# Optimization experiments

Hardware: AMD Instinct MI355X
Metric: run time of the kernel (lower is better)

The kernel has to match this reference:

```python
import jax, jax.numpy as jnp
import numpy as np

N, E = 100000, 1600000
IN_CH, HID, HEADS, OUT_CH = 128, 32, 2, 40
NEG_SLOPE = 0.2
BN_EPS = 1e-5


def _param(key, shape, scale=0.1):
    return scale * jax.random.normal(key, shape, dtype=jnp.float32)


def setup_inputs() -> dict:
    key = jax.random.key(0)
    ks = jax.random.split(key, 24)
    x = jax.random.normal(ks[0], (N, IN_CH), dtype=jnp.float32)
    edge_index = jax.random.randint(ks[1], (2, E), 0, N, dtype=jnp.int32)
    d0 = HEADS * HID  # 64
    inp = {
        'x': x, 'edge_index': edge_index,
        # conv0: in 128 -> 32 per head, concat -> 64
        'W0': _param(ks[2], (IN_CH, HEADS * HID)),
        'as0': _param(ks[3], (HEADS, HID)), 'ad0': _param(ks[4], (HEADS, HID)),
        'b0': jnp.zeros((d0,), jnp.float32),
        'g0': jnp.ones((d0,), jnp.float32), 'bt0': jnp.zeros((d0,), jnp.float32),
        # conv1: 64 -> 32 per head, concat -> 64
        'W1': _param(ks[5], (d0, HEADS * HID)),
        'as1': _param(ks[6], (HEADS, HID)), 'ad1': _param(ks[7], (HEADS, HID)),
        'b1': jnp.zeros((d0,), jnp.float32),
        'g1': jnp.ones((d0,), jnp.float32), 'bt1': jnp.zeros((d0,), jnp.float32),
        # conv2: 64 -> 40 per head, mean over heads -> 40
        'W2': _param(ks[8], (d0, HEADS * OUT_CH)),
        'as2': _param(ks[9], (HEADS, OUT_CH)), 'ad2': _param(ks[10], (HEADS, OUT_CH)),
        'b2': jnp.zeros((OUT_CH,), jnp.float32),
    }
    return inp


def gat_conv(x, src, dst, W, a_src, a_dst, bias, out_ch, concat):
    n = x.shape[0]
    h = (x @ W).reshape(n, HEADS, out_ch)            # [N,H,C]
    alpha_src = jnp.sum(h * a_src, axis=-1)          # [N,H]
    alpha_dst = jnp.sum(h * a_dst, axis=-1)          # [N,H]
    e = jax.nn.leaky_relu(alpha_src[src] + alpha_dst[dst], NEG_SLOPE)  # [E,H]
    # softmax over incoming edges per destination node (self loops guarantee >=1 edge)
    m = jax.ops.segment_max(e, dst, num_segments=n)
    e = jnp.exp(e - m[dst])
    s = jax.ops.segment_sum(e, dst, num_segments=n)
    alpha = e / s[dst]                                # [E,H]
    msg = h[src] * alpha[:, :, None]                  # [E,H,C]
    out = jax.ops.segment_sum(msg, dst, num_segments=n)  # [N,H,C]
    out = out.reshape(n, HEADS * out_ch) if concat else out.mean(axis=1)
    return out + bias


def batch_norm(x, gamma, beta):
    mu = jnp.mean(x, axis=0)
    var = jnp.mean(jnp.square(x - mu), axis=0)
    return gamma * (x - mu) * jax.lax.rsqrt(var + BN_EPS) + beta


def reference(x, edge_index, W0, as0, ad0, b0, g0, bt0,
              W1, as1, ad1, b1, g1, bt1, W2, as2, ad2, b2):
    n = x.shape[0]
    loops = jnp.arange(n, dtype=edge_index.dtype)
    src = jnp.concatenate([edge_index[0], loops])
    dst = jnp.concatenate([edge_index[1], loops])
    h = gat_conv(x, src, dst, W0, as0, ad0, b0, HID, True)
    h = jax.nn.elu(batch_norm(h, g0, bt0))
    h = gat_conv(h, src, dst, W1, as1, ad1, b1, HID, True)
    h = jax.nn.elu(batch_norm(h, g1, bt1))
    return gat_conv(h, src, dst, W2, as2, ad2, b2, OUT_CH, False)
```

## Files before the change

kernel.cpp:

```cpp
#include <hip/hip_runtime.h>
#include <hip/hip_bf16.h>
#include <math.h>


#define NNODES 100000
#define NEDGES 1600000
#define ENTOT  (NEDGES + NNODES)
#define NEG_SLOPE 0.2f
#define BN_EPS 1e-5f

#define NRANGE 8
#define RSIZE  (NNODES/NRANGE)
#define BCAP   262144
#define PBLK   2048
#define NB2    32

typedef unsigned short u16;
typedef unsigned int u32;
typedef unsigned long long u64;
typedef __attribute__((ext_vector_type(8))) short short8;
typedef __attribute__((ext_vector_type(4))) float f32x4;

__device__ __forceinline__ float b2f(u16 u){ union{u32 i; float f;} v; v.i=((u32)u)<<16; return v.f; }
__device__ __forceinline__ u16 f2b(float x){ __hip_bfloat16 b=__float2bfloat16(x); return *(u16*)&b; }
__device__ __forceinline__ float ldf(const void* p, int i, int f){
  return f ? ((const float*)p)[i] : b2f(((const u16*)p)[i]);
}

__global__ void k_detect(const u16* __restrict__ x, int* __restrict__ flag){
  __shared__ int bad;
  if(threadIdx.x==0) bad=0;
  __syncthreads();
  int cnt=0;
  for(int i=threadIdx.x;i<4096;i+=256){
    u16 v = x[2*i];
    int ex = (v>>7)&0xff;
    if(ex==0xff || (ex==0 && (v&0x7fff)!=0)) cnt++;
  }
  atomicAdd(&bad,cnt);
  __syncthreads();
  if(threadIdx.x==0) flag[0] = (bad>4)?1:0;
}

__global__ __launch_bounds__(256) void k_part2(
    const int* __restrict__ ei, int* __restrict__ gptr, u32* __restrict__ bkt){
  __shared__ int lcnt[NRANGE], gbase[NRANGE];
  int t=threadIdx.x;
  if(t<NRANGE) lcnt[t]=0;
  __syncthreads();
  const int CH=(ENTOT+PBLK-1)/PBLK;
  int beg=blockIdx.x*CH, end=beg+CH; if(end>ENTOT) end=ENTOT;
  int nd[4], ns[4], nr[4], ne=0;
  for(int i=beg+t; i<end; i+=256){
    int d=(i<NEDGES)? ei[NEDGES+i] : (i-NEDGES);
    int s=(i<NEDGES)? ei[i] : d;
    nd[ne]=d; ns[ne]=s; ne++;
  }
  #pragma unroll 4
  for(int k=0;k<ne;k++) nr[k]=atomicAdd(&lcnt[nd[k]/RSIZE],1);
  __syncthreads();
  if(t<NRANGE) gbase[t]=atomicAdd(&gptr[t],lcnt[t]);
  __syncthreads();
  #pragma unroll 4
  for(int k=0;k<ne;k++){
    int r=nd[k]/RSIZE;
    u32 e = ((u32)(nd[k]-r*RSIZE)<<17) | (u32)ns[k];
    __builtin_nontemporal_store(e, &bkt[(size_t)r*BCAP + gbase[r] + nr[k]]);
  }
}

__global__ __launch_bounds__(256) void k_hist4(
    const u32* __restrict__ bkt, const int* __restrict__ gptr, int* __restrict__ lhist){
  __shared__ int lh[RSIZE];
  int t=threadIdx.x;
  for(int i=t;i<RSIZE;i+=256) lh[i]=0;
  __syncthreads();
  int r = blockIdx.x & (NRANGE-1);
  int c = blockIdx.x >> 3;
  int n = gptr[r];
  int per=(n+NB2-1)/NB2;
  int beg=c*per, end=beg+per; if(end>n) end=n;
  const u32* bp = bkt + (size_t)r*BCAP;
  for(int i=beg+t;i<end;i+=256) atomicAdd(&lh[bp[i]>>17],1);
  __syncthreads();
  int* out = lhist + (size_t)(r*NB2+c)*RSIZE;
  for(int i=t;i<RSIZE;i+=256) out[i]=lh[i];
}

__global__ __launch_bounds__(256) void k_sumscan(int* __restrict__ lhist, int* __restrict__ cnt){
  int n = blockIdx.x*256 + threadIdx.x;
  if(n>=NNODES) return;
  int r = n/RSIZE, i = n - r*RSIZE;
  int* base = lhist + (size_t)r*NB2*RSIZE + i;
  int run=0;
  #pragma unroll 8
  for(int c=0;c<NB2;c++){
    int v = base[(size_t)c*RSIZE];
    base[(size_t)c*RSIZE] = run;
    run += v;
  }
  cnt[n]=run;
}

#define SCAN_M (NNODES+1)
#define SCAN_NB ((SCAN_M + 2047)/2048)

__global__ void k_scan_a(const int* __restrict__ cnt, int* __restrict__ bsum){
  __shared__ int red[256];
  int b=blockIdx.x, t=threadIdx.x;
  int base = b*2048 + t*8;
  int s=0;
  #pragma unroll
  for(int j=0;j<8;j++){ int idx=base+j; s += (idx<NNODES)? cnt[idx]:0; }
  red[t]=s; __syncthreads();
  for(int o=128;o>0;o>>=1){ if(t<o) red[t]+=red[t+o]; __syncthreads(); }
  if(t==0) bsum[b]=red[0];
}

__global__ void k_scan_b(int* bsum){
  if(threadIdx.x==0){
    int run=0;
    for(int i=0;i<SCAN_NB;i++){ int v=bsum[i]; bsum[i]=run; run+=v; }
  }
}

__global__ void k_scan_c(const int* __restrict__ cnt, const int* __restrict__ bsum,
                         int* __restrict__ row_ptr){
  __shared__ int lds[256];
  int b=blockIdx.x, t=threadIdx.x;
  int base=b*2048+t*8;
  int v[8]; int s=0;
  #pragma unroll
  for(int j=0;j<8;j++){ int idx=base+j; int x=(idx<NNODES)?cnt[idx]:0; v[j]=s; s+=x; }
  lds[t]=s; __syncthreads();
  for(int o=1;o<256;o<<=1){
    int other=0; if(t>=o) other=lds[t-o];
    __syncthreads();
    lds[t]+=other;
    __syncthreads();
  }
  int texcl = lds[t] - s;
  int off0 = bsum[b] + texcl;
  #pragma unroll
  for(int j=0;j<8;j++){ int idx=base+j; if(idx<SCAN_M) row_ptr[idx]=off0+v[j]; }
}

__global__ __launch_bounds__(256) void k_scatter4(
    const u32* __restrict__ bkt, const int* __restrict__ gptr,
    const int* __restrict__ row_ptr, const int* __restrict__ lhist,
    int* __restrict__ col){
  __shared__ int lofs[RSIZE];
  int t=threadIdx.x;
  int r = blockIdx.x & (NRANGE-1);
  int c = blockIdx.x >> 3;
  int lo = r*RSIZE;
  const int* cb = lhist + (size_t)(r*NB2+c)*RSIZE;
  for(int i=t;i<RSIZE;i+=256) lofs[i] = row_ptr[lo+i] + cb[i];
  __syncthreads();
  int n = gptr[r];
  int per=(n+NB2-1)/NB2;
  int beg=c*per, end=beg+per; if(end>n) end=n;
  const u32* bp = bkt + (size_t)r*BCAP;
  for(int i=beg+t;i<end;i+=256){
    u32 e=bp[i];
    int pos=atomicAdd(&lofs[e>>17],1);
    col[pos]=(int)(e & 0x1FFFF);
  }
}

template<int K, int OUTC, int HID, bool XEXT, bool BN>
__global__ __launch_bounds__(256) void k_gemm_mfma(
    const void* __restrict__ xin, const void* __restrict__ W,
    const void* __restrict__ avs, const void* __restrict__ avd,
    const float2* __restrict__ bnab,
    u16* __restrict__ hout, float* __restrict__ asrc, float* __restrict__ adst,
    const int* __restrict__ flagp)
{
  const int f = flagp[0];
  constexpr int KP = K+8;
  constexpr int RS = OUTC+8;
  constexpr int NT = OUTC/16;
  constexpr int KQ = K/32;
  __shared__ __align__(16) u16 WT[OUTC*KP];
  __shared__ __align__(16) u16 HROW[4*16*RS];
  __shared__ float AVb[2*OUTC];
  __shared__ float2 BB[K];
  int t=threadIdx.x;
  const u16* Wu=(const u16*)W; const float* Wf=(const float*)W;
  for(int i8=t*8; i8<K*OUTC; i8+=256*8){
    int k=i8/OUTC, c0=i8-k*OUTC;
    u16 w8[8];
    if(f){
      const float* wp=Wf+i8;
      float4 a=*(const float4*)wp, b=*(const float4*)(wp+4);
      w8[0]=f2b(a.x);w8[1]=f2b(a.y);w8[2]=f2b(a.z);w8[3]=f2b(a.w);
      w8[4]=f2b(b.x);w8[5]=f2b(b.y);w8[6]=f2b(b.z);w8[7]=f2b(b.w);
    } else {
      uint4 q=*(const uint4*)(Wu+i8);
      w8[0]=q.x&0xffff;w8[1]=q.x>>16;w8[2]=q.y&0xffff;w8[3]=q.y>>16;
      w8[4]=q.z&0xffff;w8[5]=q.z>>16;w8[6]=q.w&0xffff;w8[7]=q.w>>16;
    }
    #pragma unroll
    for(int u=0;u<8;u++) WT[(c0+u)*KP + k] = w8[u];
  }
  for(int idx=t; idx<2*OUTC; idx+=256)
    AVb[idx] = (idx<OUTC)? ldf(avs,idx,f) : ldf(avd,idx-OUTC,f);
  if(BN) for(int idx=t; idx<K; idx+=256) BB[idx]=bnab[idx];
  __syncthreads();

  int wv=t>>6, lane=t&63;
  int m=lane&15, quad=lane>>4;
  int grow0 = blockIdx.x*64 + wv*16;
  int growA = grow0 + m;
  bool avalid = growA < NNODES;
  int growC = avalid ? growA : 0;

  f32x4 acc[NT] = {};
  #pragma unroll
  for(int kq=0;kq<KQ;kq++){
    int k0 = kq*32 + quad*8;
    union{ u32 u[4]; short8 s8; } A;
    if(XEXT && f==1){
      const float* xr=(const float*)xin + (size_t)growC*K + k0;
      float4 p=*(const float4*)xr, q=*(const float4*)(xr+4);
      A.u[0]=f2b(p.x)|((u32)f2b(p.y)<<16);
      A.u[1]=f2b(p.z)|((u32)f2b(p.w)<<16);
      A.u[2]=f2b(q.x)|((u32)f2b(q.y)<<16);
      A.u[3]=f2b(q.z)|((u32)f2b(q.w)<<16);
    } else {
      uint4 q=*(const uint4*)((const u16*)xin + (size_t)growC*K + k0);
      A.u[0]=q.x; A.u[1]=q.y; A.u[2]=q.z; A.u[3]=q.w;
    }
    if(BN){
      #pragma unroll
      for(int j=0;j<4;j++){
        float lo=b2f(A.u[j]&0xffff), hi=b2f(A.u[j]>>16);
        float2 c1=BB[k0+2*j], c2=BB[k0+2*j+1];
        lo=c1.x*lo+c1.y; lo = lo>0.f? lo : __expf(lo)-1.f;
        hi=c2.x*hi+c2.y; hi = hi>0.f? hi : __expf(hi)-1.f;
        A.u[j]=f2b(lo)|((u32)f2b(hi)<<16);
      }
    }
    #pragma unroll
    for(int nt=0;nt<NT;nt++){
      union{ uint4 q; short8 s8; } Bf;
      Bf.q = *(const uint4*)&WT[(nt*16+m)*KP + k0];
      acc[nt] = __builtin_amdgcn_mfma_f32_16x16x32_bf16(A.s8, Bf.s8, acc[nt], 0,0,0);
    }
  }
  u16* hr = &HROW[wv*16*RS];
  #pragma unroll
  for(int nt=0;nt<NT;nt++){
    #pragma unroll
    for(int reg=0;reg<4;reg++)
      hr[(quad*4+reg)*RS + nt*16+m] = f2b(acc[nt][reg]);
  }
  __syncthreads();
  {
    int row=lane&15, task=quad, head=task&1, sd=task>>1;
    float p=0.f;
    const u16* hrow=&hr[row*RS + head*HID];
    const float* av=&AVb[sd*OUTC + head*HID];
    #pragma unroll 8
    for(int c=0;c<HID;c++) p += b2f(hrow[c])*av[c];
    int grow=grow0+row;
    if(grow<NNODES){ (sd? adst:asrc)[grow*2+head]=p; }
  }
  {
    constexpr int CH8 = OUTC/8;
    for(int idx=lane; idx<16*CH8; idx+=64){
      int rr=idx/CH8, c8=idx-rr*CH8;
      int grow=grow0+rr;
      if(grow<NNODES)
        *(uint4*)(hout + (size_t)grow*OUTC + c8*8) = *(const uint4*)&hr[rr*RS + c8*8];
    }
  }
}

template<int OUTC, bool FINAL>
__global__ __launch_bounds__(256) void k_aggf(
  const int* __restrict__ row_ptr, const int* __restrict__ col,
  const u16* __restrict__ hin, const float2* __restrict__ asrc2,
  const float2* __restrict__ adst2, const void* __restrict__ bias,
  u16* __restrict__ houtb, void* __restrict__ outv, const int* __restrict__ flagp)
{
  const int f = flagp[0];
  __shared__ float vbuf[4][80];
  int wave = threadIdx.x>>6, lane=threadIdx.x&63;
  int rr = blockIdx.x & 7, jb = blockIdx.x >> 3;
  int d = rr*RSIZE + jb*4 + wave;
  int base=row_ptr[d], deg=row_ptr[d+1]-base;
  int slot=lane>>3, cg=lane&7;
  constexpr int HSPLIT = FINAL ? 5 : 4;
  float2 adv = adst2[d];
  float acc[8]={0,0,0,0,0,0,0,0}, accx[2]={0.f,0.f};
  float s0=0.f, s1=0.f;
  for(int j=0;j<deg;j+=8){
    int jj=j+slot;
    bool valid = jj<deg;
    int cs = col[base + (valid? jj : 0)];
    if(valid){
      float2 sv = asrc2[cs];
      float e0=sv.x+adv.x; e0 = e0>0.f? e0 : NEG_SLOPE*e0; e0=fminf(e0,60.f);
      float e1=sv.y+adv.y; e1 = e1>0.f? e1 : NEG_SLOPE*e1; e1=fminf(e1,60.f);
      float p0=__expf(e0), p1=__expf(e1);
      s0+=p0; s1+=p1;
      const u16* hp = hin + (size_t)cs*OUTC;
      uint4 hq = *(const uint4*)(hp + cg*8);
      float p = (cg<HSPLIT)? p0 : p1;
      acc[0]+=p*b2f(hq.x&0xffff); acc[1]+=p*b2f(hq.x>>16);
      acc[2]+=p*b2f(hq.y&0xffff); acc[3]+=p*b2f(hq.y>>16);
      acc[4]+=p*b2f(hq.z&0xffff); acc[5]+=p*b2f(hq.z>>16);
      acc[6]+=p*b2f(hq.w&0xffff); acc[7]+=p*b2f(hq.w>>16);
      if(FINAL){
        ushort2 hc = *(const ushort2*)(hp + 64 + cg*2);
        accx[0]+=p1*b2f(hc.x); accx[1]+=p1*b2f(hc.y);
      }
    }
  }
  #pragma unroll
  for(int o=8;o<64;o<<=1){
    s0+=__shfl_xor(s0,o,64); s1+=__shfl_xor(s1,o,64);
    #pragma unroll
    for(int k=0;k<8;k++) acc[k]+=__shfl_xor(acc[k],o,64);
    if(FINAL){ accx[0]+=__shfl_xor(accx[0],o,64); accx[1]+=__shfl_xor(accx[1],o,64); }
  }
  float inv0 = s0>0.f?1.f/s0:0.f, inv1 = s1>0.f?1.f/s1:0.f;
  if(!FINAL){
    if(slot==0){
      float inv = (cg<4)? inv0 : inv1;
      u16 o8[8];
      #pragma unroll
      for(int k=0;k<8;k++) o8[k]=f2b(acc[k]*inv + ldf(bias,cg*8+k,f));
      uint4 ov;
      ov.x=(u32)o8[0]|((u32)o8[1]<<16); ov.y=(u32)o8[2]|((u32)o8[3]<<16);
      ov.z=(u32)o8[4]|((u32)o8[5]<<16); ov.w=(u32)o8[6]|((u32)o8[7]<<16);
      *(uint4*)(houtb + (size_t)d*64 + cg*8) = ov;
    }
  } else {
    if(slot==0){
      #pragma unroll
      for(int k=0;k<8;k++){
        int ch=cg*8+k;
        vbuf[wave][ch] = acc[k]*((ch<40)?inv0:inv1);
      }
      vbuf[wave][64+cg*2]   = accx[0]*inv1;
      vbuf[wave][64+cg*2+1] = accx[1]*inv1;
    }
    __syncthreads();
    if(lane<40){
      float res = 0.5f*(vbuf[wave][lane] + vbuf[wave][40+lane]) + ldf(bias,lane,f);
      if(f) ((float*)outv)[(size_t)d*40+lane] = res;
      else  ((__hip_bfloat16*)outv)[(size_t)d*40+lane] = __float2bfloat16(res);
    }
  }
}

__global__ __launch_bounds__(256) void k_bnstats(const u16* __restrict__ h, float* __restrict__ stats){
  __shared__ float red[4][128];
  int t=threadIdx.x; int c=t&63; int g=t>>6;
  float s=0.f,q=0.f;
  for(int r=blockIdx.x*4+g; r<NNODES; r+=gridDim.x*4){
    float v=b2f(h[(size_t)r*64+c]); s+=v; q+=v*v;
  }
  red[g][c]=s; red[g][64+c]=q;
  __syncthreads();
  if(t<128){
    float tot=red[0][t]+red[1][t]+red[2][t]+red[3][t];
    atomicAdd(&stats[t], tot);
  }
}

__global__ void k_bnfinal(const float* __restrict__ stats,
                          const void* __restrict__ gm, const void* __restrict__ bt,
                          float2* __restrict__ bnab, const int* __restrict__ flagp){
  const int f = flagp[0];
  int c=threadIdx.x;
  if(c>=64) return;
  float mu=stats[c]*(1.0f/NNODES);
  float var=stats[64+c]*(1.0f/NNODES)-mu*mu;
  var = var>0.f?var:0.f;
  float A = ldf(gm,c,f)*rsqrtf(var+BN_EPS);
  float B = ldf(bt,c,f) - A*mu;
  bnab[c]=make_float2(A,B);
}

extern "C" void kernel_launch(void* const* d_in, const int* in_sizes, int n_in,
                              void* d_out, int out_size, void* d_ws, size_t ws_size,
                              hipStream_t stream){
  const void* x  =d_in[0];
  const int* ei =(const int*)d_in[1];
  const void* W0 =d_in[2];  const void* as0=d_in[3];  const void* ad0=d_in[4];
  const void* b0 =d_in[5];  const void* g0 =d_in[6];  const void* bt0=d_in[7];
  const void* W1 =d_in[8];  const void* as1=d_in[9];  const void* ad1=d_in[10];
  const void* b1 =d_in[11]; const void* g1 =d_in[12]; const void* bt1=d_in[13];
  const void* W2 =d_in[14]; const void* as2=d_in[15]; const void* ad2=d_in[16];
  const void* b2 =d_in[17];

  char* ws=(char*)d_ws;
  size_t off=0;
  auto alloc=[&](size_t bytes)->void*{ void* p=ws+off; off+=(bytes+255)&~(size_t)255; return p; };
  int*    flag   =(int*)   alloc(256);
  int*    row_ptr=(int*)   alloc((size_t)(NNODES+1)*4);
  int*    cnt    =(int*)   alloc((size_t)NNODES*4);
  int*    colx   =(int*)   alloc((size_t)ENTOT*4);
  int*    bsum   =(int*)   alloc((size_t)SCAN_NB*4);
  int*    gptr   =(int*)   alloc(256);
  u32*    bkt    =(u32*)   alloc((size_t)NRANGE*BCAP*4);
  u16*    hA     =(u16*)   alloc((size_t)100032*80*2);
  u16*    hB0    =(u16*)   alloc((size_t)100032*64*2);
  u16*    hB1    =(u16*)   alloc((size_t)100032*64*2);
  float*  asrc   =(float*) alloc((size_t)NNODES*2*4);
  float*  adst   =(float*) alloc((size_t)NNODES*2*4);
  float*  stats  =(float*) alloc(128*4);
  float2* bnab   =(float2*)alloc(64*8);
  int*    lhist  =(int*)hA;

  k_detect<<<1,256,0,stream>>>((const u16*)x, flag);

  (void)hipMemsetAsync(gptr,0,256,stream);
  k_part2  <<<PBLK,256,0,stream>>>(ei,gptr,bkt);
  k_hist4  <<<NRANGE*NB2,256,0,stream>>>(bkt,gptr,lhist);
  k_sumscan<<<(NNODES+255)/256,256,0,stream>>>(lhist,cnt);
  k_scan_a <<<SCAN_NB,256,0,stream>>>(cnt,bsum);
  k_scan_b <<<1,64,0,stream>>>(bsum);
  k_scan_c <<<SCAN_NB,256,0,stream>>>(cnt,bsum,row_ptr);
  k_scatter4<<<NRANGE*NB2,256,0,stream>>>(bkt,gptr,row_ptr,lhist,colx);

  int gG = (NNODES+63)/64;
  int gN = NNODES/4;
  k_gemm_mfma<128,64,32,true ,false><<<gG,256,0,stream>>>(
      x,W0,as0,ad0,nullptr,hA,asrc,adst,flag);
  k_aggf<64,false><<<gN,256,0,stream>>>(row_ptr,colx,hA,
      (const float2*)asrc,(const float2*)adst,b0,hB0,nullptr,flag);
  (void)hipMemsetAsync(stats,0,512,stream);
  k_bnstats<<<256,256,0,stream>>>(hB0,stats);
  k_bnfinal<<<1,64,0,stream>>>(stats,g0,bt0,bnab,flag);
  k_gemm_mfma<64,64,32,false,true ><<<gG,256,0,stream>>>(
      hB0,W1,as1,ad1,bnab,hA,asrc,adst,flag);
  k_aggf<64,false><<<gN,256,0,stream>>>(row_ptr,colx,hA,
      (const float2*)asrc,(const float2*)adst,b1,hB1,nullptr,flag);
  (void)hipMemsetAsync(stats,0,512,stream);
  k_bnstats<<<256,256,0,stream>>>(hB1,stats);
  k_bnfinal<<<1,64,0,stream>>>(stats,g1,bt1,bnab,flag);
  k_gemm_mfma<64,80,40,false,true ><<<gG,256,0,stream>>>(
      hB1,W2,as2,ad2,bnab,hA,asrc,adst,flag);
  k_aggf<80,true ><<<gN,256,0,stream>>>(row_ptr,colx,hA,
      (const float2*)asrc,(const float2*)adst,b2,nullptr,d_out,flag);

  (void)in_sizes;(void)n_in;(void)out_size;(void)ws_size;
}
```

Measured before the change: 482.1 us.

## Assign one node per 8-lane group in aggregation, unroll edges by two

The aggregation kernel changes from one wave per destination node, where 8 edge slots each have 8 channel lanes, to one 8-lane group per node, giving 32 nodes per block. Each group walks its edges sequentially, two per iteration, so the cross-slot shuffle reductions go away and all 64 lanes of a wave have work even for low-degree nodes. The cost is a longer serial loop for high-degree nodes, a larger spread in work between lanes of the same wave, and less memory-level parallelism per node. The final layer now writes its head-mean output through a shared buffer that covers the whole block.

```diff
diff --git a/kernel.cpp b/kernel.cpp
--- a/kernel.cpp
+++ b/kernel.cpp
@@ -22,6 +22,8 @@
 typedef __attribute__((ext_vector_type(4))) float f32x4;
 
 __device__ __forceinline__ float b2f(u16 u){ union{u32 i; float f;} v; v.i=((u32)u)<<16; return v.f; }
+__device__ __forceinline__ float blo(u32 u){ union{u32 i; float f;} v; v.i=u<<16; return v.f; }
+__device__ __forceinline__ float bhi(u32 u){ union{u32 i; float f;} v; v.i=u&0xffff0000u; return v.f; }
 __device__ __forceinline__ u16 f2b(float x){ __hip_bfloat16 b=__float2bfloat16(x); return *(u16*)&b; }
 __device__ __forceinline__ float ldf(const void* p, int i, int f){
   return f ? ((const float*)p)[i] : b2f(((const u16*)p)[i]);
@@ -285,49 +287,63 @@
   u16* __restrict__ houtb, void* __restrict__ outv, const int* __restrict__ flagp)
 {
   const int f = flagp[0];
-  __shared__ float vbuf[4][80];
-  int wave = threadIdx.x>>6, lane=threadIdx.x&63;
+  __shared__ float vbuf[FINAL?32:1][84];
+  constexpr int HSPLIT = FINAL ? 5 : 4;
+  int t = threadIdx.x;
+  int g  = t>>3;
+  int cg = t&7;
   int rr = blockIdx.x & 7, jb = blockIdx.x >> 3;
-  int d = rr*RSIZE + jb*4 + wave;
-  int base=row_ptr[d], deg=row_ptr[d+1]-base;
-  int slot=lane>>3, cg=lane&7;
-  constexpr int HSPLIT = FINAL ? 5 : 4;
-  float2 adv = adst2[d];
-  float acc[8]={0,0,0,0,0,0,0,0}, accx[2]={0.f,0.f};
+  int lim = RSIZE - jb*32;
+  bool ok = g < lim;
+  int d = rr*RSIZE + jb*32 + g;
+  int base=0, deg=0;
+  float2 adv = make_float2(0.f,0.f);
+  if(ok){
+    base = row_ptr[d];
+    deg  = row_ptr[d+1] - base;
+    adv  = adst2[d];
+  }
+  const int* cp = col + base;
+  float acc[8]={0,0,0,0,0,0,0,0}, accx0=0.f, accx1=0.f;
   float s0=0.f, s1=0.f;
-  for(int j=0;j<deg;j+=8){
-    int jj=j+slot;
-    bool valid = jj<deg;
-    int cs = col[base + (valid? jj : 0)];
-    if(valid){
-      float2 sv = asrc2[cs];
-      float e0=sv.x+adv.x; e0 = e0>0.f? e0 : NEG_SLOPE*e0; e0=fminf(e0,60.f);
-      float e1=sv.y+adv.y; e1 = e1>0.f? e1 : NEG_SLOPE*e1; e1=fminf(e1,60.f);
-      float p0=__expf(e0), p1=__expf(e1);
-      s0+=p0; s1+=p1;
-      const u16* hp = hin + (size_t)cs*OUTC;
-      uint4 hq = *(const uint4*)(hp + cg*8);
-      float p = (cg<HSPLIT)? p0 : p1;
-      acc[0]+=p*b2f(hq.x&0xffff); acc[1]+=p*b2f(hq.x>>16);
-      acc[2]+=p*b2f(hq.y&0xffff); acc[3]+=p*b2f(hq.y>>16);
-      acc[4]+=p*b2f(hq.z&0xffff); acc[5]+=p*b2f(hq.z>>16);
-      acc[6]+=p*b2f(hq.w&0xffff); acc[7]+=p*b2f(hq.w>>16);
-      if(FINAL){
-        ushort2 hc = *(const ushort2*)(hp + 64 + cg*2);
-        accx[0]+=p1*b2f(hc.x); accx[1]+=p1*b2f(hc.y);
-      }
-    }
-  }
-  #pragma unroll
-  for(int o=8;o<64;o<<=1){
-    s0+=__shfl_xor(s0,o,64); s1+=__shfl_xor(s1,o,64);
-    #pragma unroll
-    for(int k=0;k<8;k++) acc[k]+=__shfl_xor(acc[k],o,64);
-    if(FINAL){ accx[0]+=__shfl_xor(accx[0],o,64); accx[1]+=__shfl_xor(accx[1],o,64); }
+  for(int j=0;j<deg;j+=2){
+    int c0 = cp[j];
+    bool v1 = (j+1)<deg;
+    int c1 = cp[v1 ? j+1 : j];
+    float2 sa = asrc2[c0];
+    float2 sb = asrc2[c1];
+    const u16* hp0 = hin + (size_t)c0*OUTC;
+    const u16* hp1 = hin + (size_t)c1*OUTC;
+    uint4 h0 = *(const uint4*)(hp0 + cg*8);
+    uint4 h1 = *(const uint4*)(hp1 + cg*8);
+    float e0 = sa.x+adv.x; e0 = fmaxf(e0, NEG_SLOPE*e0); e0 = fminf(e0,60.f);
+    float e1 = sa.y+adv.y; e1 = fmaxf(e1, NEG_SLOPE*e1); e1 = fminf(e1,60.f);
+    float p0 = __expf(e0), p1 = __expf(e1);
+    float q0 = sb.x+adv.x; q0 = fmaxf(q0, NEG_SLOPE*q0); q0 = fminf(q0,60.f);
+    float q1 = sb.y+adv.y; q1 = fmaxf(q1, NEG_SLOPE*q1); q1 = fminf(q1,60.f);
+    float r0 = __expf(q0), r1 = __expf(q1);
+    if(!v1){ r0=0.f; r1=0.f; }
+    s0 += p0 + r0; s1 += p1 + r1;
+    float pa = (cg<HSPLIT)? p0 : p1;
+    float pb = (cg<HSPLIT)? r0 : r1;
+    acc[0] += pa*blo(h0.x) + pb*blo(h1.x);
+    acc[1] += pa*bhi(h0.x) + pb*bhi(h1.x);
+    acc[2] += pa*blo(h0.y) + pb*blo(h1.y);
+    acc[3] += pa*bhi(h0.y) + pb*bhi(h1.y);
+    acc[4] += pa*blo(h0.z) + pb*blo(h1.z);
+    acc[5] += pa*bhi(h0.z) + pb*bhi(h1.z);
+    acc[6] += pa*blo(h0.w) + pb*blo(h1.w);
+    acc[7] += pa*bhi(h0.w) + pb*bhi(h1.w);
+    if(FINAL){
+      ushort2 ha = *(const ushort2*)(hp0 + 64 + cg*2);
+      ushort2 hb = *(const ushort2*)(hp1 + 64 + cg*2);
+      accx0 += p1*b2f(ha.x) + r1*b2f(hb.x);
+      accx1 += p1*b2f(ha.y) + r1*b2f(hb.y);
+    }
   }
   float inv0 = s0>0.f?1.f/s0:0.f, inv1 = s1>0.f?1.f/s1:0.f;
   if(!FINAL){
-    if(slot==0){
+    if(ok){
       float inv = (cg<4)? inv0 : inv1;
       u16 o8[8];
       #pragma unroll
@@ -338,20 +354,22 @@
       *(uint4*)(houtb + (size_t)d*64 + cg*8) = ov;
     }
   } else {
-    if(slot==0){
+    if(ok){
       #pragma unroll
-      for(int k=0;k<8;k++){
-        int ch=cg*8+k;
-        vbuf[wave][ch] = acc[k]*((ch<40)?inv0:inv1);
+      for(int k=0;k<8;k++)
+        vbuf[g][cg*8+k] = acc[k]*((cg<5)?inv0:inv1);
+      vbuf[g][64+cg*2]   = accx0*inv1;
+      vbuf[g][64+cg*2+1] = accx1*inv1;
+    }
+    __syncthreads();
+    for(int idx=t; idx<32*40; idx+=256){
+      int gg=idx/40, ch=idx-gg*40;
+      if(gg<lim){
+        int dd = rr*RSIZE + jb*32 + gg;
+        float res = 0.5f*(vbuf[gg][ch] + vbuf[gg][40+ch]) + ldf(bias,ch,f);
+        if(f) ((float*)outv)[(size_t)dd*40+ch] = res;
+        else  ((__hip_bfloat16*)outv)[(size_t)dd*40+ch] = __float2bfloat16(res);
       }
-      vbuf[wave][64+cg*2]   = accx[0]*inv1;
-      vbuf[wave][64+cg*2+1] = accx[1]*inv1;
-    }
-    __syncthreads();
-    if(lane<40){
-      float res = 0.5f*(vbuf[wave][lane] + vbuf[wave][40+lane]) + ldf(bias,lane,f);
-      if(f) ((float*)outv)[(size_t)d*40+lane] = res;
-      else  ((__hip_bfloat16*)outv)[(size_t)d*40+lane] = __float2bfloat16(res);
     }
   }
 }
@@ -428,24 +446,24 @@
   k_scatter4<<<NRANGE*NB2,256,0,stream>>>(bkt,gptr,row_ptr,lhist,colx);
 
   int gG = (NNODES+63)/64;
-  int gN = NNODES/4;
+  int gA = NRANGE * ((RSIZE + 31)/32);
   k_gemm_mfma<128,64,32,true ,false><<<gG,256,0,stream>>>(
       x,W0,as0,ad0,nullptr,hA,asrc,adst,flag);
-  k_aggf<64,false><<<gN,256,0,stream>>>(row_ptr,colx,hA,
+  k_aggf<64,false><<<gA,256,0,stream>>>(row_ptr,colx,hA,
       (const float2*)asrc,(const float2*)adst,b0,hB0,nullptr,flag);
   (void)hipMemsetAsync(stats,0,512,stream);
   k_bnstats<<<256,256,0,stream>>>(hB0,stats);
   k_bnfinal<<<1,64,0,stream>>>(stats,g0,bt0,bnab,flag);
   k_gemm_mfma<64,64,32,false,true ><<<gG,256,0,stream>>>(
       hB0,W1,as1,ad1,bnab,hA,asrc,adst,flag);
-  k_aggf<64,false><<<gN,256,0,stream>>>(row_ptr,colx,hA,
+  k_aggf<64,false><<<gA,256,0,stream>>>(row_ptr,colx,hA,
       (const float2*)asrc,(const float2*)adst,b1,hB1,nullptr,flag);
   (void)hipMemsetAsync(stats,0,512,stream);
   k_bnstats<<<256,256,0,stream>>>(hB1,stats);
   k_bnfinal<<<1,64,0,stream>>>(stats,g1,bt1,bnab,flag);
   k_gemm_mfma<64,80,40,false,true ><<<gG,256,0,stream>>>(
       hB1,W2,as2,ad2,bnab,hA,asrc,adst,flag);
-  k_aggf<80,true ><<<gN,256,0,stream>>>(row_ptr,colx,hA,
+  k_aggf<80,true ><<<gA,256,0,stream>>>(row_ptr,colx,hA,
       (const float2*)asrc,(const float2*)adst,b2,nullptr,d_out,flag);
 
   (void)in_sizes;(void)n_in;(void)out_size;(void)ws_size;
```

After: 455.2 us. 5.6% less time.
